# Optimization experiments

Hardware: AMD Instinct MI355X
Metric: run time of the kernel (lower is better)

The kernel has to match this reference:

```python
import jax, jax.numpy as jnp
import numpy as np
from jax import lax

VOCAB = 32000
EMBED = 1024
HIDDEN = 1024
ML = 64          # config.MAX_LENGTH
L = 50           # input sentence length
HH = HIDDEN // 2 # per-direction encoder hidden


def _lstm_cell(x, h, c, Wih, Whh, bih, bhh):
    # torch LSTM gate order: i, f, g, o
    g = x @ Wih.T + h @ Whh.T + bih + bhh
    i, f, gg, o = jnp.split(g, 4)
    i = jax.nn.sigmoid(i)
    f = jax.nn.sigmoid(f)
    gg = jnp.tanh(gg)
    o = jax.nn.sigmoid(o)
    c = f * c + i * gg
    return o * jnp.tanh(c), c


def setup_inputs() -> dict:
    key = jax.random.key(0)
    ks = jax.random.split(key, 24)
    def n(k, shape, s=0.05):
        return jax.random.normal(k, shape, jnp.float32) * s
    return {
        "x_tokens": jax.random.randint(ks[0], (L,), 0, VOCAB, jnp.int32),
        "allowed_mask": jnp.ones((VOCAB + ML,), jnp.float32),
        "embedding": n(ks[1], (VOCAB, EMBED)),
        # encoder bi-LSTM (two cells, each hidden//2)
        "Wih_f": n(ks[2], (4 * HH, EMBED)), "Whh_f": n(ks[3], (4 * HH, HH)),
        "bih_f": n(ks[4], (4 * HH,)), "bhh_f": n(ks[5], (4 * HH,)),
        "Wih_b": n(ks[6], (4 * HH, EMBED)), "Whh_b": n(ks[7], (4 * HH, HH)),
        "bih_b": n(ks[8], (4 * HH,)), "bhh_b": n(ks[9], (4 * HH,)),
        # decoder LSTM: input = embed + 2*hidden
        "Wih_d": n(ks[10], (4 * HIDDEN, EMBED + 2 * HIDDEN)),
        "Whh_d": n(ks[11], (4 * HIDDEN, HIDDEN)),
        "bih_d": n(ks[12], (4 * HIDDEN,)), "bhh_d": n(ks[13], (4 * HIDDEN,)),
        # attention: Linear(2*hidden -> MAX_LENGTH)
        "attn_W": n(ks[14], (ML, 2 * HIDDEN)), "attn_b": n(ks[15], (ML,)),
        # generate layer: Linear(hidden -> vocab)
        "gen_W": n(ks[16], (VOCAB, HIDDEN)), "gen_b": n(ks[17], (VOCAB,)),
        # copy layer: Linear(hidden -> hidden)
        "copy_W": n(ks[18], (HIDDEN, HIDDEN)), "copy_b": n(ks[19], (HIDDEN,)),
    }


def _forward(allowed_mask, embedding, Wih_f, Whh_f, bih_f, bhh_f,
             Wih_b, Whh_b, bih_b, bhh_b, Wih_d, Whh_d, bih_d, bhh_d,
             attn_W, attn_b, gen_W, gen_b, copy_W, copy_b, x_tokens):
    xemb = embedding[x_tokens]  # (L, EMBED)

    # --- encoder: two LSTM cells both stepped forward-in-time (as in the
    # original, where the bidirectional LSTM is called one token at a time) ---
    def enc_step(carry, xe):
        hf, cf, hb, cb = carry
        hf, cf = _lstm_cell(xe, hf, cf, Wih_f, Whh_f, bih_f, bhh_f)
        hb, cb = _lstm_cell(xe, hb, cb, Wih_b, Whh_b, bih_b, bhh_b)
        return (hf, cf, hb, cb), jnp.concatenate([hf, hb])

    z = jnp.zeros((HH,), xemb.dtype)
    (hf, cf, hb, cb), enc = lax.scan(enc_step, (z, z, z, z), xemb)
    enc_outs = jnp.zeros((ML, HIDDEN), xemb.dtype).at[:L].set(enc)  # padded buffer
    h0 = jnp.concatenate([hf, hb])  # (HIDDEN,) decoder init
    c0 = jnp.concatenate([cf, cb])

    copy_enc = jnp.tanh(enc_outs @ copy_W.T + copy_b)  # (ML, HIDDEN), loop-invariant
    pos = jnp.arange(ML)
    sent_pad = jnp.full((ML,), -1, jnp.int32).at[:L].set(x_tokens)
    sos_emb = embedding[0]

    def dec_step(carry, t):
        h, c, prev_probs, prev_word, dec_in = carry
        first = t == 0
        # attentive read
        a = jnp.concatenate([dec_in, h])  # (2*HIDDEN,)
        attw = jax.nn.softmax(a @ attn_W.T + attn_b)
        attentive = attw @ enc_outs  # (HIDDEN,)
        # selective (copy) read from previous step's copy probs
        pc = prev_probs[VOCAB:]
        m = ((pos >= 1) & (pos < L - 1) & (sent_pad != prev_word)).astype(pc.dtype)
        pc = pc * m
        s = pc.sum()
        pc = jnp.where(s > 0, pc / jnp.where(s > 0, s, 1.0), pc)
        selective = pc @ enc_outs
        zero = jnp.zeros_like(attentive)
        attentive = jnp.where(first, zero, attentive)
        selective = jnp.where(first, zero, selective)
        # decoder LSTM step
        h, c = _lstm_cell(jnp.concatenate([dec_in, selective, attentive]),
                          h, c, Wih_d, Whh_d, bih_d, bhh_d)
        gen = h @ gen_W.T + gen_b        # (VOCAB,)
        copy = copy_enc @ h              # (ML,)
        probs = jax.nn.softmax(jnp.concatenate([gen, copy]))
        dist = probs * allowed_mask
        # deterministic action (argmax in place of Categorical.sample)
        aidx = jnp.argmax(dist)
        is_voc = aidx < VOCAB
        src = sent_pad[jnp.clip(aidx - VOCAB, 0, L - 1)]
        action = jnp.where(is_voc, aidx, src).astype(jnp.int32)
        prob = dist[aidx] + jnp.where(
            is_voc, jnp.zeros((), dist.dtype), dist[jnp.clip(action, 0, VOCAB - 1)])
        new = (h, c, lax.stop_gradient(probs), action, embedding[action])
        return new, (h, prob, action)

    carry0 = (h0, c0, jnp.zeros((VOCAB + ML,), h0.dtype),
              jnp.array(-1, jnp.int32), sos_emb)
    _, (hs, probs, actions) = lax.scan(dec_step, carry0, jnp.arange(ML))
    states = jnp.concatenate([h0[None], hs])  # (ML+1, HIDDEN)
    return states, probs, actions


def reference(x_tokens, allowed_mask, embedding, Wih_f, Whh_f, bih_f, bhh_f,
              Wih_b, Whh_b, bih_b, bhh_b, Wih_d, Whh_d, bih_d, bhh_d,
              attn_W, attn_b, gen_W, gen_b, copy_W, copy_b):
    return _forward(allowed_mask, embedding, Wih_f, Whh_f, bih_f, bhh_f,
                    Wih_b, Whh_b, bih_b, bhh_b, Wih_d, Whh_d, bih_d, bhh_d,
                    attn_W, attn_b, gen_W, gen_b, copy_W, copy_b, x_tokens)
```

## Files before the change

kernel.cpp:

```cpp
#include <hip/hip_runtime.h>
#include <math.h>

#define L 50
#define ML 64
#define VOCAB 32000
#define EMBED 1024
#define HID 1024
#define HH 512
#define TOT (VOCAB+ML)
#define NPART 501

#define WS_ENC_GATES 0
#define WS_C_ENC     8192
#define WS_ENC_OUTS  10240
#define WS_COPY_ENC  75776
#define WS_H_DEC     141312
#define WS_C_DEC     143360
#define WS_X_DEC     145408
#define WS_DGATES    148480
#define WS_LOGITS    152576
#define WS_PARTS     184640
#define WS_ATTW      186688
#define WS_PC        186752
#define WS_ACT       186816
#define WS_G         186880
#define WS_G_END     (186880+8192*64)
#define WS_PREG      711168
#define WS_END       (711168+50*4096)

__device__ __forceinline__ float wred_sum(float v){
  #pragma unroll
  for(int o=32;o;o>>=1) v += __shfl_xor(v,o,64);
  return v;
}
__device__ __forceinline__ float wred_max(float v){
  #pragma unroll
  for(int o=32;o;o>>=1) v = fmaxf(v,__shfl_xor(v,o,64));
  return v;
}
__device__ __forceinline__ float sigm(float x){ return 1.0f/(1.0f+__expf(-x)); }
__device__ __forceinline__ float d4(float4 a, float4 b){ return a.x*b.x + a.y*b.y + a.z*b.z + a.w*b.w; }

__global__ __launch_bounds__(256) void k_enc_pre2(
  const int* __restrict__ xt, const float* __restrict__ emb,
  const float* __restrict__ Wih_f, const float* __restrict__ bih_f, const float* __restrict__ bhh_f,
  const float* __restrict__ Wih_b, const float* __restrict__ bih_b, const float* __restrict__ bhh_b,
  float* __restrict__ ws)
{
  __shared__ int toks[L];
  const int tid=threadIdx.x, b=blockIdx.x, wave=tid>>6, lane=tid&63;
  float* pg = ws + WS_PREG;
  if(tid<L) toks[tid]=xt[tid];
  float4 wih[2][4]; float bias[2];
  #pragma unroll
  for(int rr=0;rr<2;rr++){
    int r=b*8+wave*2+rr; bool isF=(r<2048); int rl=isF?r:(r-2048);
    const float* wp=(isF?Wih_f:Wih_b)+(size_t)rl*EMBED;
    #pragma unroll
    for(int c4=0;c4<4;c4++) wih[rr][c4]=*(const float4*)(wp+c4*256+lane*4);
    bias[rr]= isF?(bih_f[rl]+bhh_f[rl]):(bih_b[rl]+bhh_b[rl]);
  }
  __syncthreads();
  for(int t=0;t<L;t++){
    const float* er = emb + (size_t)toks[t]*EMBED;
    #pragma unroll
    for(int rr=0;rr<2;rr++){
      int r=b*8+wave*2+rr;
      float acc=0.0f;
      #pragma unroll
      for(int c4=0;c4<4;c4++) acc += d4(wih[rr][c4], *(const float4*)(er + c4*256 + lane*4));
      acc=wred_sum(acc);
      if(lane==0) pg[(size_t)t*4096+r]=acc+bias[rr];
    }
  }
}

__global__ __launch_bounds__(256) void k_enc_rec(
  const float* __restrict__ Whh_f, const float* __restrict__ Whh_b,
  float* __restrict__ ws, int t)
{
  __shared__ __align__(16) float h_lds[1024];
  const int tid=threadIdx.x, b=blockIdx.x, wave=tid>>6, lane=tid&63;
  float* gates   = ws + WS_ENC_GATES;
  float* c_enc   = ws + WS_C_ENC;
  float* enc_outs= ws + WS_ENC_OUTS;
  const float* pg = ws + WS_PREG + (size_t)t*4096;
  if(t>0){
    const float* gp = gates + ((t-1)&1)*4096;
    const float* cp = c_enc + (t&1)*1024;
    float* cw = c_enc + ((t-1)&1)*1024;
    for(int u=tid;u<1024;u+=256){
      int base=(u<512)?0:2048, uu=(u<512)?u:(u-512);
      float ig=gp[base+uu], fg=gp[base+512+uu], gg=gp[base+1024+uu], og=gp[base+1536+uu];
      float cprev=(t==1)?0.0f:cp[u];
      float c=sigm(fg)*cprev+sigm(ig)*tanhf(gg);
      float h=sigm(og)*tanhf(c);
      h_lds[u]=h;
      if(b==0){ cw[u]=c; enc_outs[(size_t)(t-1)*1024+u]=h; }
    }
  }
  __syncthreads();
  float* gw = gates + (t&1)*4096;
  #pragma unroll
  for(int rr=0;rr<2;rr++){
    int r=b*8+wave*2+rr; bool isF=(r<2048); int rl=isF?r:(r-2048);
    if(t==0){
      if(lane==0) gw[r]=pg[r];
    } else {
      const float* hr=(isF?Whh_f:Whh_b)+(size_t)rl*HH;
      const float* hs=&h_lds[isF?0:512];
      float acc=0.0f;
      #pragma unroll
      for(int c2=0;c2<2;c2++){
        int m=c2*256+lane*4;
        acc += d4(*(const float4*)(hr+m), *(const float4*)(&hs[m]));
      }
      acc=wred_sum(acc);
      if(lane==0) gw[r]=pg[r]+acc;
    }
  }
}

__global__ __launch_bounds__(256) void k_enc_step(
  const int* __restrict__ xt, const float* __restrict__ emb,
  const float* __restrict__ Wih_f, const float* __restrict__ Whh_f,
  const float* __restrict__ bih_f, const float* __restrict__ bhh_f,
  const float* __restrict__ Wih_b, const float* __restrict__ Whh_b,
  const float* __restrict__ bih_b, const float* __restrict__ bhh_b,
  float* __restrict__ ws, int t)
{
  __shared__ __align__(16) float h_lds[1024];
  __shared__ __align__(16) float xe[1024];
  const int tid = threadIdx.x;
  float* gates   = ws + WS_ENC_GATES;
  float* c_enc   = ws + WS_C_ENC;
  float* enc_outs= ws + WS_ENC_OUTS;
  {
    const int tok = xt[t];
    const float* er = emb + (size_t)tok*EMBED;
    for(int j=tid;j<1024;j+=256) xe[j]=er[j];
  }
  if(t>0){
    const float* gp = gates + ((t-1)&1)*4096;
    const float* cp = c_enc + (t&1)*1024;
    float* cw = c_enc + ((t-1)&1)*1024;
    for(int u=tid;u<1024;u+=256){
      int base=(u<512)?0:2048, uu=(u<512)?u:(u-512);
      float ig=gp[base+uu], fg=gp[base+512+uu], gg=gp[base+1024+uu], og=gp[base+1536+uu];
      float cprev=(t==1)?0.0f:cp[u];
      float c=sigm(fg)*cprev+sigm(ig)*tanhf(gg);
      float h=sigm(og)*tanhf(c);
      h_lds[u]=h;
      if(blockIdx.x==0){ cw[u]=c; enc_outs[(size_t)(t-1)*1024+u]=h; }
    }
  }
  __syncthreads();
  float* gw = gates + (t&1)*4096;
  const int wave=tid>>6, lane=tid&63;
  for(int rr=0;rr<2;rr++){
    int r=blockIdx.x*8+wave*2+rr;
    bool isF=(r<2048); int rl=isF?r:(r-2048);
    const float* Wih=isF?Wih_f:Wih_b;
    const float* Whh=isF?Whh_f:Whh_b;
    float bias=isF?(bih_f[rl]+bhh_f[rl]):(bih_b[rl]+bhh_b[rl]);
    const float* wr=Wih+(size_t)rl*EMBED;
    float acc=0.0f;
    #pragma unroll
    for(int c4=0;c4<4;c4++){
      int m=c4*256+lane*4;
      acc += d4(*(const float4*)(wr+m), *(const float4*)(&xe[m]));
    }
    if(t>0){
      const float* hr=Whh+(size_t)rl*HH;
      const float* hs=&h_lds[isF?0:512];
      #pragma unroll
      for(int c2=0;c2<2;c2++){
        int m=c2*256+lane*4;
        acc += d4(*(const float4*)(hr+m), *(const float4*)(&hs[m]));
      }
    }
    acc=wred_sum(acc);
    if(lane==0) gw[r]=acc+bias;
  }
}

__global__ __launch_bounds__(256) void k_copy_final(
  const float* __restrict__ emb,
  const float* __restrict__ copy_W, const float* __restrict__ copy_b,
  float* __restrict__ ws, float* __restrict__ out)
{
  __shared__ __align__(16) float hf[1024];
  const int tid=threadIdx.x, b=blockIdx.x, wave=tid>>6, lane=tid&63;
  float* gates = ws + WS_ENC_GATES;
  float* c_enc = ws + WS_C_ENC;
  float* enc_outs = ws + WS_ENC_OUTS;
  float* cenc = ws + WS_COPY_ENC;
  float* h_dec = ws + WS_H_DEC;
  float* c_dec = ws + WS_C_DEC;
  float* x_dec = ws + WS_X_DEC;
  {
    const float* gp = gates + ((L-1)&1)*4096;
    const float* cp = c_enc + ((L-2)&1)*1024;
    for(int u=tid;u<1024;u+=256){
      int base=(u<512)?0:2048, uu=(u<512)?u:(u-512);
      float ig=gp[base+uu], fg=gp[base+512+uu], gg=gp[base+1024+uu], og=gp[base+1536+uu];
      float c=sigm(fg)*cp[u]+sigm(ig)*tanhf(gg);
      float h=sigm(og)*tanhf(c);
      hf[u]=h;
      if(b==0){
        enc_outs[(size_t)(L-1)*1024+u]=h;
        h_dec[1024+u]=h;
        c_dec[1024+u]=c;
        out[u]=h;
      }
    }
    if(b==1) for(int j=tid;j<(ML-L)*1024;j+=256) enc_outs[(size_t)L*1024+j]=0.0f;
    if(b==2) for(int j=tid;j<1024;j+=256){
      x_dec[j]=emb[j];
      x_dec[1024+j]=0.0f;
      x_dec[2048+j]=0.0f;
    }
  }
  __syncthreads();
  int j = b*4 + wave;
  const float* wr = copy_W + (size_t)j*1024;
  float4 w0=*(const float4*)(wr+0*256+lane*4);
  float4 w1=*(const float4*)(wr+1*256+lane*4);
  float4 w2=*(const float4*)(wr+2*256+lane*4);
  float4 w3=*(const float4*)(wr+3*256+lane*4);
  float bj = copy_b[j];
  for(int k=0;k<L-1;k++){
    const float* er = enc_outs + (size_t)k*1024;
    float acc = d4(w0,*(const float4*)(er+0*256+lane*4))
              + d4(w1,*(const float4*)(er+1*256+lane*4))
              + d4(w2,*(const float4*)(er+2*256+lane*4))
              + d4(w3,*(const float4*)(er+3*256+lane*4));
    acc = wred_sum(acc);
    if(lane==0) cenc[(size_t)k*1024+j]=tanhf(acc+bj);
  }
  {
    float acc = d4(w0,*(const float4*)(&hf[0*256+lane*4]))
              + d4(w1,*(const float4*)(&hf[1*256+lane*4]))
              + d4(w2,*(const float4*)(&hf[2*256+lane*4]))
              + d4(w3,*(const float4*)(&hf[3*256+lane*4]));
    acc = wred_sum(acc);
    if(lane==0) cenc[(size_t)(L-1)*1024+j]=tanhf(acc+bj);
  }
  if(lane==0){
    float z=tanhf(0.0f+bj);
    for(int k=L;k<ML;k++) cenc[(size_t)k*1024+j]=z;
  }
}

__global__ __launch_bounds__(256) void k_gmat(const float* __restrict__ Wih_d, float* __restrict__ ws)
{
  __shared__ __align__(16) float elds[16*1024];
  const int tid=threadIdx.x, wave=tid>>6, lane=tid&63;
  const float* enc = ws + WS_ENC_OUTS;
  float* G = ws + WS_G;
  float4 w[4][4];
  int rg[4];
  #pragma unroll
  for(int q=0;q<4;q++){
    int r = blockIdx.x*16 + wave*4 + q;
    rg[q]=r;
    const float* W = (r<4096) ? (Wih_d + (size_t)r*3072 + 1024)
                              : (Wih_d + (size_t)(r-4096)*3072 + 2048);
    #pragma unroll
    for(int c4=0;c4<4;c4++) w[q][c4]=*(const float4*)(W + c4*256 + lane*4);
  }
  for(int chunk=0;chunk<4;chunk++){
    __syncthreads();
    for(int idx=tid; idx<16*1024; idx+=256) elds[idx]=enc[(size_t)chunk*16*1024+idx];
    __syncthreads();
    for(int k=0;k<16;k++){
      #pragma unroll
      for(int q=0;q<4;q++){
        float acc=0.0f;
        #pragma unroll
        for(int c4=0;c4<4;c4++)
          acc += d4(w[q][c4], *(const float4*)(&elds[k*1024 + c4*256 + lane*4]));
        acc=wred_sum(acc);
        if(lane==0) G[(size_t)rg[q]*64 + chunk*16 + k]=acc;
      }
    }
  }
}

__global__ __launch_bounds__(256) void k_fin16(
  const int* __restrict__ xt, const float* __restrict__ amask,
  const float* __restrict__ emb,
  const float* __restrict__ attn_W, const float* __restrict__ attn_b,
  float* __restrict__ ws, float* __restrict__ out, int t, int fin_only)
{
  __shared__ __align__(16) float dec_in[1024];
  __shared__ __align__(16) float hprev[1024];
  __shared__ float r_lm[256], r_sm[256], r_ky[256];
  __shared__ int r_ix[256];
  __shared__ float s_lmax, s_Z;
  __shared__ int s_act;
  const int tid=threadIdx.x, b=blockIdx.x, wave=tid>>6, lane=tid&63;
  float* h_dec=ws+WS_H_DEC;
  float* logits=ws+WS_LOGITS; float* parts=ws+WS_PARTS;
  float* attw_raw=ws+WS_ATTW; float* pcw=ws+WS_PC;

  {
    float lm=-INFINITY, sm=0.0f, ky=-INFINITY; int ix=0x7fffffff;
    for(int i=tid;i<NPART;i+=256){
      const float4 p = *(const float4*)(parts+(size_t)i*4);
      float plm=p.x, psm=p.y, pky=p.z; int pix=__float_as_int(p.w);
      if(plm>lm){ sm = sm*__expf(lm-plm)+psm; lm=plm; }
      else sm += psm*__expf(plm-lm);
      if(pky>ky || (pky==ky && pix<ix)){ ky=pky; ix=pix; }
    }
    r_lm[tid]=lm; r_sm[tid]=sm; r_ky[tid]=ky; r_ix[tid]=ix;
    __syncthreads();
    for(int s=128;s;s>>=1){
      if(tid<s){
        float blm=r_lm[tid+s], bsm=r_sm[tid+s];
        float alm=r_lm[tid], a_sm=r_sm[tid];
        if(blm>alm){ r_sm[tid]=a_sm*__expf(alm-blm)+bsm; r_lm[tid]=blm; }
        else r_sm[tid]=a_sm+bsm*__expf(blm-alm);
        float bky=r_ky[tid+s]; int bix=r_ix[tid+s];
        if(bky>r_ky[tid] || (bky==r_ky[tid] && bix<r_ix[tid])){ r_ky[tid]=bky; r_ix[tid]=bix; }
      }
      __syncthreads();
    }
    if(tid==0){
      float lmax=r_lm[0]; float Z=r_sm[0];
      float bky=r_ky[0];
      int aidx = (bky==-INFINITY)?0:r_ix[0];
      bool isv = aidx<VOCAB;
      int kcl = aidx-VOCAB; kcl = kcl<0?0:(kcl>(L-1)?(L-1):kcl);
      int sp = xt[kcl];
      int action = isv? aidx : sp;
      if(b==0){
        float prob = amask[aidx]*__expf(logits[aidx]-lmax)/Z;
        if(!isv){
          int a2 = action<0?0:(action>(VOCAB-1)?(VOCAB-1):action);
          prob += amask[a2]*__expf(logits[a2]-lmax)/Z;
        }
        out[65*1024 + (t-1)] = prob;
        out[65*1024 + 64 + (t-1)] = (float)action;
        *(int*)(ws+WS_ACT) = action;
      }
      s_lmax=lmax; s_Z=Z; s_act=action;
    }
  }
  __syncthreads();
  if(fin_only) return;

  const int action = s_act;
  if(b==0 && tid<64){
    int k=tid;
    float v=__expf(logits[VOCAB+k]-s_lmax)/s_Z;
    int sp=(k<L)? xt[k] : -1;
    float m=(k>=1 && k<(L-1) && sp!=action)?1.0f:0.0f;
    float pv=v*m;
    float s=wred_sum(pv);
    pcw[k]=(s>0.0f)? pv/s : pv;
  }
  {
    int row = action<0 ? action+VOCAB : action;
    const float* er = emb + (size_t)row*EMBED;
    const float* hp = h_dec + ((t-1)&1)*1024;
    for(int j=tid;j<1024;j+=256){ dec_in[j]=er[j]; hprev[j]=hp[j]; }
  }
  __syncthreads();
  {
    int r = b*4 + wave;
    const float* wr = attn_W + (size_t)r*2048;
    float acc=0.0f;
    #pragma unroll
    for(int c4=0;c4<4;c4++){
      int m=c4*256+lane*4;
      acc += d4(*(const float4*)(wr+m),      *(const float4*)(&dec_in[m]));
      acc += d4(*(const float4*)(wr+1024+m), *(const float4*)(&hprev[m]));
    }
    acc=wred_sum(acc);
    if(lane==0) attw_raw[r]=acc+attn_b[r];
  }
}

__global__ __launch_bounds__(256) void k_dec_gates3(
  const float* __restrict__ emb,
  const float* __restrict__ Wih_d, const float* __restrict__ Whh_d,
  const float* __restrict__ bih_d, const float* __restrict__ bhh_d,
  float* __restrict__ ws, int t)
{
  __shared__ __align__(16) float di[1024];
  __shared__ __align__(16) float hh[1024];
  __shared__ float pcs[64], aws[64];
  const int tid=threadIdx.x;
  float* h_dec=ws+WS_H_DEC; float* dg=ws+WS_DGATES;
  const float* G=ws+WS_G;
  if(t==0){
    for(int j=tid;j<1024;j+=256) di[j]=emb[j];
    if(tid<64){ pcs[tid]=0.0f; aws[tid]=0.0f; }
  } else {
    const int action = *(const int*)(ws+WS_ACT);
    const float* er = emb + (size_t)action*EMBED;
    for(int j=tid;j<1024;j+=256) di[j]=er[j];
    if(tid<64){
      pcs[tid]=(ws+WS_PC)[tid];
      float v=(ws+WS_ATTW)[tid];
      float mx=wred_max(v);
      float e=__expf(v-mx);
      float s=wred_sum(e);
      aws[tid]=e/s;
    }
  }
  {
    const float* hp=h_dec+((t+1)&1)*1024;
    for(int j=tid;j<1024;j+=256) hh[j]=hp[j];
  }
  __syncthreads();
  const int wave=tid>>6, lane=tid&63;
  for(int rr=0;rr<2;rr++){
    int r=blockIdx.x*8+wave*2+rr;
    const float* wd=Wih_d+(size_t)r*3072;
    float acc=0.0f;
    #pragma unroll
    for(int c4=0;c4<4;c4++){
      int m=c4*256+lane*4;
      acc += d4(*(const float4*)(wd+m), *(const float4*)(&di[m]));
    }
    const float* hr=Whh_d+(size_t)r*1024;
    #pragma unroll
    for(int c4=0;c4<4;c4++){
      int m=c4*256+lane*4;
      acc += d4(*(const float4*)(hr+m), *(const float4*)(&hh[m]));
    }
    acc += G[(size_t)r*64+lane]*pcs[lane];
    acc += G[(size_t)(4096+r)*64+lane]*aws[lane];
    acc=wred_sum(acc);
    if(lane==0) dg[r]=acc+bih_d[r]+bhh_d[r];
  }
}

__global__ __launch_bounds__(256) void k_dec_init(const float* __restrict__ emb, float* __restrict__ ws)
{
  float* x_dec=ws+WS_X_DEC;
  for(int j=threadIdx.x;j<1024;j+=256){
    x_dec[j]=emb[j];
    x_dec[1024+j]=0.0f;
    x_dec[2048+j]=0.0f;
  }
}

__global__ __launch_bounds__(256) void k_attn(
  const int* __restrict__ xt, const float* __restrict__ amask,
  const float* __restrict__ emb,
  const float* __restrict__ attn_W, const float* __restrict__ attn_b,
  float* __restrict__ ws, float* __restrict__ out, int t, int fin_only)
{
  __shared__ __align__(16) float dec_in[1024];
  __shared__ __align__(16) float hprev[1024];
  __shared__ float r_lm[256], r_sm[256], r_ky[256];
  __shared__ int r_ix[256];
  __shared__ float s_lmax, s_Z;
  __shared__ int s_act;
  const int tid=threadIdx.x;
  float* h_dec=ws+WS_H_DEC; float* x_dec=ws+WS_X_DEC;
  float* logits=ws+WS_LOGITS; float* parts=ws+WS_PARTS;
  float* attw_raw=ws+WS_ATTW; float* pcw=ws+WS_PC;
  {
    float lm=-INFINITY, sm=0.0f, ky=-INFINITY; int ix=0x7fffffff;
    for(int i=tid;i<NPART;i+=256){
      const float4 p = *(const float4*)(parts+(size_t)i*4);
      float plm=p.x, psm=p.y, pky=p.z; int pix=__float_as_int(p.w);
      if(plm>lm){ sm = sm*__expf(lm-plm)+psm; lm=plm; }
      else sm += psm*__expf(plm-lm);
      if(pky>ky || (pky==ky && pix<ix)){ ky=pky; ix=pix; }
    }
    r_lm[tid]=lm; r_sm[tid]=sm; r_ky[tid]=ky; r_ix[tid]=ix;
    __syncthreads();
    for(int s=128;s;s>>=1){
      if(tid<s){
        float blm=r_lm[tid+s], bsm=r_sm[tid+s];
        float alm=r_lm[tid], a_sm=r_sm[tid];
        if(blm>alm){ r_sm[tid]=a_sm*__expf(alm-blm)+bsm; r_lm[tid]=blm; }
        else r_sm[tid]=a_sm+bsm*__expf(blm-alm);
        float bky=r_ky[tid+s]; int bix=r_ix[tid+s];
        if(bky>r_ky[tid] || (bky==r_ky[tid] && bix<r_ix[tid])){ r_ky[tid]=bky; r_ix[tid]=bix; }
      }
      __syncthreads();
    }
    if(tid==0){
      float lmax=r_lm[0]; float Z=r_sm[0];
      float bky=r_ky[0];
      int aidx = (bky==-INFINITY)?0:r_ix[0];
      bool isv = aidx<VOCAB;
      int kcl = aidx-VOCAB; kcl = kcl<0?0:(kcl>(L-1)?(L-1):kcl);
      int sp = xt[kcl];
      int action = isv? aidx : sp;
      if(blockIdx.x==0){
        float prob = amask[aidx]*__expf(logits[aidx]-lmax)/Z;
        if(!isv){
          int a2 = action<0?0:(action>(VOCAB-1)?(VOCAB-1):action);
          prob += amask[a2]*__expf(logits[a2]-lmax)/Z;
        }
        out[65*1024 + (t-1)] = prob;
        out[65*1024 + 64 + (t-1)] = (float)action;
      }
      s_lmax=lmax; s_Z=Z; s_act=action;
    }
  }
  __syncthreads();
  if(fin_only) return;
  const int action = s_act;
  if(blockIdx.x==0 && tid<64){
    int k=tid;
    float v=__expf(logits[VOCAB+k]-s_lmax)/s_Z;
    int sp=(k<L)? xt[k] : -1;
    float m=(k>=1 && k<(L-1) && sp!=action)?1.0f:0.0f;
    float pv=v*m;
    float s=wred_sum(pv);
    pcw[k]=(s>0.0f)? pv/s : pv;
  }
  {
    int row = action<0 ? action+VOCAB : action;
    const float* er = emb + (size_t)row*EMBED;
    const float* hp = h_dec + ((t-1)&1)*1024;
    for(int j=tid;j<1024;j+=256){
      float v=er[j];
      dec_in[j]=v; hprev[j]=hp[j];
      if(blockIdx.x==0) x_dec[j]=v;
    }
  }
  __syncthreads();
  if(tid<64){
    const int lane=tid;
    const float* wr = attn_W + (size_t)blockIdx.x*2048;
    float acc=0.0f;
    #pragma unroll
    for(int c4=0;c4<4;c4++){
      int m=c4*256+lane*4;
      acc += d4(*(const float4*)(wr+m),      *(const float4*)(&dec_in[m]));
      acc += d4(*(const float4*)(wr+1024+m), *(const float4*)(&hprev[m]));
    }
    acc=wred_sum(acc);
    if(lane==0) attw_raw[blockIdx.x]=acc+attn_b[blockIdx.x];
  }
}

__global__ __launch_bounds__(256) void k_prep(float* __restrict__ ws)
{
  __shared__ float attw_s[64], pc_s[64];
  const int tid=threadIdx.x;
  float* enc_outs=ws+WS_ENC_OUTS; float* x_dec=ws+WS_X_DEC;
  float* attw_raw=ws+WS_ATTW; float* pcw=ws+WS_PC;
  if(tid<64){
    float v=attw_raw[tid];
    float mx=wred_max(v);
    float e=__expf(v-mx);
    float s=wred_sum(e);
    attw_s[tid]=e/s;
    pc_s[tid]=pcw[tid];
  }
  __syncthreads();
  int j=blockIdx.x*256+tid;
  float aA=0.0f, aS=0.0f;
  for(int k=0;k<ML;k++){
    float e=enc_outs[(size_t)k*1024+j];
    aA += attw_s[k]*e;
    aS += pc_s[k]*e;
  }
  x_dec[1024+j]=aS;
  x_dec[2048+j]=aA;
}

__global__ __launch_bounds__(256) void k_dec_gates(
  const float* __restrict__ Wih_d, const float* __restrict__ Whh_d,
  const float* __restrict__ bih_d, const float* __restrict__ bhh_d,
  float* __restrict__ ws, int t)
{
  __shared__ __align__(16) float x_lds[4096];
  const int tid=threadIdx.x;
  float* x_dec=ws+WS_X_DEC; float* h_dec=ws+WS_H_DEC; float* dg=ws+WS_DGATES;
  for(int j=tid;j<3072;j+=256) x_lds[j]=x_dec[j];
  {
    const float* hp=h_dec+((t+1)&1)*1024;
    for(int j=tid;j<1024;j+=256) x_lds[3072+j]=hp[j];
  }
  __syncthreads();
  const int wave=tid>>6, lane=tid&63;
  for(int rr=0;rr<2;rr++){
    int r=blockIdx.x*8+wave*2+rr;
    const float* wr=Wih_d+(size_t)r*3072;
    float acc=0.0f;
    #pragma unroll
    for(int c4=0;c4<12;c4++){
      int m=c4*256+lane*4;
      acc += d4(*(const float4*)(wr+m), *(const float4*)(&x_lds[m]));
    }
    const float* hr=Whh_d+(size_t)r*1024;
    #pragma unroll
    for(int c4=0;c4<4;c4++){
      int m=c4*256+lane*4;
      acc += d4(*(const float4*)(hr+m), *(const float4*)(&x_lds[3072+m]));
    }
    acc=wred_sum(acc);
    if(lane==0) dg[r]=acc+bih_d[r]+bhh_d[r];
  }
}

__global__ __launch_bounds__(256) void k_dec_gen(
  const float* __restrict__ gen_W, const float* __restrict__ gen_b,
  const float* __restrict__ amask,
  float* __restrict__ ws, float* __restrict__ out, int t)
{
  __shared__ __align__(16) float h_lds[1024];
  __shared__ float w_lm[4], w_sm[4], w_ky[4];
  __shared__ int w_ix[4];
  const int tid=threadIdx.x;
  float* dg=ws+WS_DGATES;
  float* c_dec=ws+WS_C_DEC; float* h_dec=ws+WS_H_DEC;
  float* logits=ws+WS_LOGITS; float* parts=ws+WS_PARTS;
  float* cenc=ws+WS_COPY_ENC;
  {
    const float* cp=c_dec+((t+1)&1)*1024;
    float* cw=c_dec+(t&1)*1024;
    float* hw=h_dec+(t&1)*1024;
    for(int u=tid;u<1024;u+=256){
      float ig=dg[u], fg=dg[1024+u], gg=dg[2048+u], og=dg[3072+u];
      float c=sigm(fg)*cp[u]+sigm(ig)*tanhf(gg);
      float h=sigm(og)*tanhf(c);
      h_lds[u]=h;
      if(blockIdx.x==0){ cw[u]=c; hw[u]=h; out[(size_t)(t+1)*1024+u]=h; }
    }
  }
  __syncthreads();
  const int wave=tid>>6, lane=tid&63;
  const int b=blockIdx.x;
  const bool isGen=(b<500);
  const int rbase = isGen ? (b*64+wave*16) : (VOCAB+wave*16);
  float lv[16];
  #pragma unroll
  for(int rr=0;rr<16;rr++){
    const float* wr = isGen ? gen_W+(size_t)(rbase+rr)*1024
                            : cenc +(size_t)(rbase-VOCAB+rr)*1024;
    float acc=0.0f;
    #pragma unroll
    for(int c4=0;c4<4;c4++){
      int m=c4*256+lane*4;
      acc += d4(*(const float4*)(wr+m), *(const float4*)(&h_lds[m]));
    }
    acc=wred_sum(acc);
    lv[rr] = isGen ? acc+gen_b[rbase+rr] : acc;
  }
  if(lane==0){
    float lm=-INFINITY, ky=-INFINITY; int ix=0;
    #pragma unroll
    for(int rr=0;rr<16;rr++){
      int gi=rbase+rr;
      logits[gi]=lv[rr];
      lm=fmaxf(lm,lv[rr]);
      float mk=amask[gi];
      float kk = (mk>0.0f)? (lv[rr]+__logf(mk)) : -INFINITY;
      if(kk>ky){ ky=kk; ix=gi; }
    }
    float sm=0.0f;
    #pragma unroll
    for(int rr=0;rr<16;rr++) sm += __expf(lv[rr]-lm);
    w_lm[wave]=lm; w_sm[wave]=sm; w_ky[wave]=ky; w_ix[wave]=ix;
  }
  __syncthreads();
  if(tid==0){
    float lm=w_lm[0], sm=w_sm[0], ky=w_ky[0]; int ix=w_ix[0];
    for(int w=1;w<4;w++){
      float blm=w_lm[w], bsm=w_sm[w];
      if(blm>lm){ sm=sm*__expf(lm-blm)+bsm; lm=blm; }
      else sm += bsm*__expf(blm-lm);
      if(w_ky[w]>ky || (w_ky[w]==ky && w_ix[w]<ix)){ ky=w_ky[w]; ix=w_ix[w]; }
    }
    float4 p; p.x=lm; p.y=sm; p.z=ky; p.w=__int_as_float(ix);
    *(float4*)(parts+(size_t)blockIdx.x*4)=p;
  }
}

extern "C" void kernel_launch(void* const* d_in, const int* in_sizes, int n_in,
                              void* d_out, int out_size, void* d_ws, size_t ws_size,
                              hipStream_t stream)
{
  const int*   xt     = (const int*)d_in[0];
  const float* amask  = (const float*)d_in[1];
  const float* emb    = (const float*)d_in[2];
  const float* Wih_f  = (const float*)d_in[3];
  const float* Whh_f  = (const float*)d_in[4];
  const float* bih_f  = (const float*)d_in[5];
  const float* bhh_f  = (const float*)d_in[6];
  const float* Wih_b  = (const float*)d_in[7];
  const float* Whh_b  = (const float*)d_in[8];
  const float* bih_b  = (const float*)d_in[9];
  const float* bhh_b  = (const float*)d_in[10];
  const float* Wih_d  = (const float*)d_in[11];
  const float* Whh_d  = (const float*)d_in[12];
  const float* bih_d  = (const float*)d_in[13];
  const float* bhh_d  = (const float*)d_in[14];
  const float* attn_W = (const float*)d_in[15];
  const float* attn_b = (const float*)d_in[16];
  const float* gen_W  = (const float*)d_in[17];
  const float* gen_b  = (const float*)d_in[18];
  const float* copy_W = (const float*)d_in[19];
  const float* copy_b = (const float*)d_in[20];
  float* out=(float*)d_out;
  float* ws =(float*)d_ws;

  const bool hasG    = ws_size >= (size_t)WS_G_END*sizeof(float);
  const bool hasPreg = ws_size >= (size_t)WS_END*sizeof(float);

  if(hasPreg){
    k_enc_pre2<<<512,256,0,stream>>>(xt,emb,Wih_f,bih_f,bhh_f,Wih_b,bih_b,bhh_b,ws);
    for(int t=0;t<L;t++)
      k_enc_rec<<<512,256,0,stream>>>(Whh_f,Whh_b,ws,t);
  } else {
    for(int t=0;t<L;t++)
      k_enc_step<<<512,256,0,stream>>>(xt,emb,Wih_f,Whh_f,bih_f,bhh_f,Wih_b,Whh_b,bih_b,bhh_b,ws,t);
  }
  k_copy_final<<<256,256,0,stream>>>(emb,copy_W,copy_b,ws,out);

  if(hasG){
    k_gmat<<<512,256,0,stream>>>(Wih_d,ws);
    k_dec_gates3<<<512,256,0,stream>>>(emb,Wih_d,Whh_d,bih_d,bhh_d,ws,0);
    k_dec_gen   <<<501,256,0,stream>>>(gen_W,gen_b,amask,ws,out,0);
    for(int t=1;t<ML;t++){
      k_fin16     <<<16,256,0,stream>>>(xt,amask,emb,attn_W,attn_b,ws,out,t,0);
      k_dec_gates3<<<512,256,0,stream>>>(emb,Wih_d,Whh_d,bih_d,bhh_d,ws,t);
      k_dec_gen   <<<501,256,0,stream>>>(gen_W,gen_b,amask,ws,out,t);
    }
    k_fin16<<<1,256,0,stream>>>(xt,amask,emb,attn_W,attn_b,ws,out,ML,1);
  } else {
    k_dec_init<<<1,256,0,stream>>>(emb,ws);
    k_dec_gates<<<512,256,0,stream>>>(Wih_d,Whh_d,bih_d,bhh_d,ws,0);
    k_dec_gen  <<<501,256,0,stream>>>(gen_W,gen_b,amask,ws,out,0);
    for(int t=1;t<ML;t++){
      k_attn     <<<64,256,0,stream>>>(xt,amask,emb,attn_W,attn_b,ws,out,t,0);
      k_prep     <<<4,256,0,stream>>>(ws);
      k_dec_gates<<<512,256,0,stream>>>(Wih_d,Whh_d,bih_d,bhh_d,ws,t);
      k_dec_gen  <<<501,256,0,stream>>>(gen_W,gen_b,amask,ws,out,t);
    }
    k_attn<<<1,256,0,stream>>>(xt,amask,emb,attn_W,attn_b,ws,out,ML,1);
  }
}
```

Before: 3.099 ms.

## Precompute attention embedding projections and fuse finalize into decoder gate kernel

Adds a one-time table P of attn_W's embedding half applied to every vocabulary embedding, so each decoder step gets its attention logits by a row lookup plus a hidden-state projection. That projection is computed by an extra block appended to the generator kernel. The argmax/softmax finalize, copy and attention softmax are folded into the gate kernel, removing the per-step finalize launch. G's padded columns are zeroed and their compute skipped. The cost is a large upfront projection over all 32000 embeddings and a big workspace requirement, with a fallback path when the workspace is too small.

```diff
diff --git a/kernel.cpp b/kernel.cpp
--- a/kernel.cpp
+++ b/kernel.cpp
@@ -26,7 +26,10 @@
 #define WS_G         186880
 #define WS_G_END     (186880+8192*64)
 #define WS_PREG      711168
-#define WS_END       (711168+50*4096)
+#define WS_PREG_END  (711168+50*4096)
+#define WS_AH        915968
+#define WS_P         916032
+#define WS_P_END     (916032+32000*64)
 
 __device__ __forceinline__ float wred_sum(float v){
   #pragma unroll
@@ -252,7 +255,7 @@
   }
 }
 
-__global__ __launch_bounds__(256) void k_gmat(const float* __restrict__ Wih_d, float* __restrict__ ws)
+__global__ __launch_bounds__(256) void k_gmat2(const float* __restrict__ Wih_d, float* __restrict__ ws)
 {
   __shared__ __align__(16) float elds[16*1024];
   const int tid=threadIdx.x, wave=tid>>6, lane=tid&63;
@@ -270,10 +273,11 @@
     for(int c4=0;c4<4;c4++) w[q][c4]=*(const float4*)(W + c4*256 + lane*4);
   }
   for(int chunk=0;chunk<4;chunk++){
+    const int nk = (chunk<3)?16:2;
     __syncthreads();
-    for(int idx=tid; idx<16*1024; idx+=256) elds[idx]=enc[(size_t)chunk*16*1024+idx];
+    for(int idx=tid; idx<nk*1024; idx+=256) elds[idx]=enc[(size_t)chunk*16*1024+idx];
     __syncthreads();
-    for(int k=0;k<16;k++){
+    for(int k=0;k<nk;k++){
       #pragma unroll
       for(int q=0;q<4;q++){
         float acc=0.0f;
@@ -283,6 +287,42 @@
         acc=wred_sum(acc);
         if(lane==0) G[(size_t)rg[q]*64 + chunk*16 + k]=acc;
       }
+    }
+  }
+  if(lane==0){
+    #pragma unroll
+    for(int q=0;q<4;q++)
+      for(int kk=50;kk<64;kk++) G[(size_t)rg[q]*64 + kk]=0.0f;
+  }
+}
+
+__global__ __launch_bounds__(1024) void k_pmat(
+  const float* __restrict__ emb, const float* __restrict__ attn_W, float* __restrict__ ws)
+{
+  __shared__ __align__(16) float xe[1024];
+  const int tid=threadIdx.x, wave=tid>>6, lane=tid&63;
+  float* P = ws + WS_P;
+  float4 w[4][4];
+  #pragma unroll
+  for(int q=0;q<4;q++){
+    int r = wave*4+q;
+    const float* wr = attn_W + (size_t)r*2048;
+    #pragma unroll
+    for(int c4=0;c4<4;c4++) w[q][c4]=*(const float4*)(wr + c4*256 + lane*4);
+  }
+  const int w0 = blockIdx.x*64;
+  for(int wv=0;wv<64;wv++){
+    __syncthreads();
+    xe[tid]=emb[(size_t)(w0+wv)*EMBED + tid];
+    __syncthreads();
+    #pragma unroll
+    for(int q=0;q<4;q++){
+      int r = wave*4+q;
+      float acc=0.0f;
+      #pragma unroll
+      for(int c4=0;c4<4;c4++) acc += d4(w[q][c4], *(const float4*)(&xe[c4*256+lane*4]));
+      acc=wred_sum(acc);
+      if(lane==0) P[(size_t)(w0+wv)*64 + r]=acc;
     }
   }
 }
@@ -303,7 +343,6 @@
   float* h_dec=ws+WS_H_DEC;
   float* logits=ws+WS_LOGITS; float* parts=ws+WS_PARTS;
   float* attw_raw=ws+WS_ATTW; float* pcw=ws+WS_PC;
-
   {
     float lm=-INFINITY, sm=0.0f, ky=-INFINITY; int ix=0x7fffffff;
     for(int i=tid;i<NPART;i+=256){
@@ -379,6 +418,120 @@
     }
     acc=wred_sum(acc);
     if(lane==0) attw_raw[r]=acc+attn_b[r];
+  }
+}
+
+__global__ __launch_bounds__(256) void k_dec_gates4(
+  const int* __restrict__ xt, const float* __restrict__ amask,
+  const float* __restrict__ emb, const float* __restrict__ attn_b,
+  const float* __restrict__ Wih_d, const float* __restrict__ Whh_d,
+  const float* __restrict__ bih_d, const float* __restrict__ bhh_d,
+  float* __restrict__ ws, float* __restrict__ out, int t)
+{
+  __shared__ __align__(16) float di[1024];
+  __shared__ __align__(16) float hh[1024];
+  __shared__ float pcs[64], aws[64];
+  __shared__ float r_lm[256], r_sm[256], r_ky[256];
+  __shared__ int r_ix[256];
+  __shared__ float s_lmax, s_Z;
+  __shared__ int s_act;
+  const int tid=threadIdx.x, b=blockIdx.x, wave=tid>>6, lane=tid&63;
+  float* h_dec=ws+WS_H_DEC; float* dg=ws+WS_DGATES;
+  float* logits=ws+WS_LOGITS; float* parts=ws+WS_PARTS;
+  const float* G=ws+WS_G;
+
+  if(t==0){
+    for(int j=tid;j<1024;j+=256) di[j]=emb[j];
+    if(tid<64){ pcs[tid]=0.0f; aws[tid]=0.0f; }
+  } else {
+    float lm=-INFINITY, sm=0.0f, ky=-INFINITY; int ix=0x7fffffff;
+    for(int i=tid;i<NPART;i+=256){
+      const float4 p = *(const float4*)(parts+(size_t)i*4);
+      float plm=p.x, psm=p.y, pky=p.z; int pix=__float_as_int(p.w);
+      if(plm>lm){ sm = sm*__expf(lm-plm)+psm; lm=plm; }
+      else sm += psm*__expf(plm-lm);
+      if(pky>ky || (pky==ky && pix<ix)){ ky=pky; ix=pix; }
+    }
+    r_lm[tid]=lm; r_sm[tid]=sm; r_ky[tid]=ky; r_ix[tid]=ix;
+    __syncthreads();
+    for(int s=128;s;s>>=1){
+      if(tid<s){
+        float blm=r_lm[tid+s], bsm=r_sm[tid+s];
+        float alm=r_lm[tid], a_sm=r_sm[tid];
+        if(blm>alm){ r_sm[tid]=a_sm*__expf(alm-blm)+bsm; r_lm[tid]=blm; }
+        else r_sm[tid]=a_sm+bsm*__expf(blm-alm);
+        float bky=r_ky[tid+s]; int bix=r_ix[tid+s];
+        if(bky>r_ky[tid] || (bky==r_ky[tid] && bix<r_ix[tid])){ r_ky[tid]=bky; r_ix[tid]=bix; }
+      }
+      __syncthreads();
+    }
+    if(tid==0){
+      float lmax=r_lm[0]; float Z=r_sm[0];
+      float bky=r_ky[0];
+      int aidx = (bky==-INFINITY)?0:r_ix[0];
+      bool isv = aidx<VOCAB;
+      int kcl = aidx-VOCAB; kcl = kcl<0?0:(kcl>(L-1)?(L-1):kcl);
+      int sp = xt[kcl];
+      int action = isv? aidx : sp;
+      if(b==0){
+        float prob = amask[aidx]*__expf(logits[aidx]-lmax)/Z;
+        if(!isv){
+          int a2 = action<0?0:(action>(VOCAB-1)?(VOCAB-1):action);
+          prob += amask[a2]*__expf(logits[a2]-lmax)/Z;
+        }
+        out[65*1024 + (t-1)] = prob;
+        out[65*1024 + 64 + (t-1)] = (float)action;
+      }
+      s_lmax=lmax; s_Z=Z; s_act=action;
+    }
+    __syncthreads();
+    const int action = s_act;
+    if(tid<64){
+      int k=tid;
+      float v=__expf(logits[VOCAB+k]-s_lmax)/s_Z;
+      int sp=(k<L)? xt[k] : -1;
+      float m=(k>=1 && k<(L-1) && sp!=action)?1.0f:0.0f;
+      float pv=v*m;
+      float s=wred_sum(pv);
+      pcs[k]=(s>0.0f)? pv/s : pv;
+    }
+    __syncthreads();
+    if(tid<64){
+      float raw = (ws+WS_P)[(size_t)action*64 + tid] + (ws+WS_AH)[tid] + attn_b[tid];
+      float mx=wred_max(raw);
+      float e=__expf(raw-mx);
+      float s=wred_sum(e);
+      aws[tid]=e/s;
+    }
+    {
+      const float* er = emb + (size_t)action*EMBED;
+      for(int j=tid;j<1024;j+=256) di[j]=er[j];
+    }
+  }
+  {
+    const float* hp=h_dec+((t+1)&1)*1024;
+    for(int j=tid;j<1024;j+=256) hh[j]=hp[j];
+  }
+  __syncthreads();
+  for(int rr=0;rr<2;rr++){
+    int r=b*8+wave*2+rr;
+    const float* wd=Wih_d+(size_t)r*3072;
+    float acc=0.0f;
+    #pragma unroll
+    for(int c4=0;c4<4;c4++){
+      int m=c4*256+lane*4;
+      acc += d4(*(const float4*)(wd+m), *(const float4*)(&di[m]));
+    }
+    const float* hr=Whh_d+(size_t)r*1024;
+    #pragma unroll
+    for(int c4=0;c4<4;c4++){
+      int m=c4*256+lane*4;
+      acc += d4(*(const float4*)(hr+m), *(const float4*)(&hh[m]));
+    }
+    acc += G[(size_t)r*64+lane]*pcs[lane];
+    acc += G[(size_t)(4096+r)*64+lane]*aws[lane];
+    acc=wred_sum(acc);
+    if(lane==0) dg[r]=acc+bih_d[r]+bhh_d[r];
   }
 }
 
@@ -438,176 +591,9 @@
   }
 }
 
-__global__ __launch_bounds__(256) void k_dec_init(const float* __restrict__ emb, float* __restrict__ ws)
-{
-  float* x_dec=ws+WS_X_DEC;
-  for(int j=threadIdx.x;j<1024;j+=256){
-    x_dec[j]=emb[j];
-    x_dec[1024+j]=0.0f;
-    x_dec[2048+j]=0.0f;
-  }
-}
-
-__global__ __launch_bounds__(256) void k_attn(
-  const int* __restrict__ xt, const float* __restrict__ amask,
-  const float* __restrict__ emb,
-  const float* __restrict__ attn_W, const float* __restrict__ attn_b,
-  float* __restrict__ ws, float* __restrict__ out, int t, int fin_only)
-{
-  __shared__ __align__(16) float dec_in[1024];
-  __shared__ __align__(16) float hprev[1024];
-  __shared__ float r_lm[256], r_sm[256], r_ky[256];
-  __shared__ int r_ix[256];
-  __shared__ float s_lmax, s_Z;
-  __shared__ int s_act;
-  const int tid=threadIdx.x;
-  float* h_dec=ws+WS_H_DEC; float* x_dec=ws+WS_X_DEC;
-  float* logits=ws+WS_LOGITS; float* parts=ws+WS_PARTS;
-  float* attw_raw=ws+WS_ATTW; float* pcw=ws+WS_PC;
-  {
-    float lm=-INFINITY, sm=0.0f, ky=-INFINITY; int ix=0x7fffffff;
-    for(int i=tid;i<NPART;i+=256){
-      const float4 p = *(const float4*)(parts+(size_t)i*4);
-      float plm=p.x, psm=p.y, pky=p.z; int pix=__float_as_int(p.w);
-      if(plm>lm){ sm = sm*__expf(lm-plm)+psm; lm=plm; }
-      else sm += psm*__expf(plm-lm);
-      if(pky>ky || (pky==ky && pix<ix)){ ky=pky; ix=pix; }
-    }
-    r_lm[tid]=lm; r_sm[tid]=sm; r_ky[tid]=ky; r_ix[tid]=ix;
-    __syncthreads();
-    for(int s=128;s;s>>=1){
-      if(tid<s){
-        float blm=r_lm[tid+s], bsm=r_sm[tid+s];
-        float alm=r_lm[tid], a_sm=r_sm[tid];
-        if(blm>alm){ r_sm[tid]=a_sm*__expf(alm-blm)+bsm; r_lm[tid]=blm; }
-        else r_sm[tid]=a_sm+bsm*__expf(blm-alm);
-        float bky=r_ky[tid+s]; int bix=r_ix[tid+s];
-        if(bky>r_ky[tid] || (bky==r_ky[tid] && bix<r_ix[tid])){ r_ky[tid]=bky; r_ix[tid]=bix; }
-      }
-      __syncthreads();
-    }
-    if(tid==0){
-      float lmax=r_lm[0]; float Z=r_sm[0];
-      float bky=r_ky[0];
-      int aidx = (bky==-INFINITY)?0:r_ix[0];
-      bool isv = aidx<VOCAB;
-      int kcl = aidx-VOCAB; kcl = kcl<0?0:(kcl>(L-1)?(L-1):kcl);
-      int sp = xt[kcl];
-      int action = isv? aidx : sp;
-      if(blockIdx.x==0){
-        float prob = amask[aidx]*__expf(logits[aidx]-lmax)/Z;
-        if(!isv){
-          int a2 = action<0?0:(action>(VOCAB-1)?(VOCAB-1):action);
-          prob += amask[a2]*__expf(logits[a2]-lmax)/Z;
-        }
-        out[65*1024 + (t-1)] = prob;
-        out[65*1024 + 64 + (t-1)] = (float)action;
-      }
-      s_lmax=lmax; s_Z=Z; s_act=action;
-    }
-  }
-  __syncthreads();
-  if(fin_only) return;
-  const int action = s_act;
-  if(blockIdx.x==0 && tid<64){
-    int k=tid;
-    float v=__expf(logits[VOCAB+k]-s_lmax)/s_Z;
-    int sp=(k<L)? xt[k] : -1;
-    float m=(k>=1 && k<(L-1) && sp!=action)?1.0f:0.0f;
-    float pv=v*m;
-    float s=wred_sum(pv);
-    pcw[k]=(s>0.0f)? pv/s : pv;
-  }
-  {
-    int row = action<0 ? action+VOCAB : action;
-    const float* er = emb + (size_t)row*EMBED;
-    const float* hp = h_dec + ((t-1)&1)*1024;
-    for(int j=tid;j<1024;j+=256){
-      float v=er[j];
-      dec_in[j]=v; hprev[j]=hp[j];
-      if(blockIdx.x==0) x_dec[j]=v;
-    }
-  }
-  __syncthreads();
-  if(tid<64){
-    const int lane=tid;
-    const float* wr = attn_W + (size_t)blockIdx.x*2048;
-    float acc=0.0f;
-    #pragma unroll
-    for(int c4=0;c4<4;c4++){
-      int m=c4*256+lane*4;
-      acc += d4(*(const float4*)(wr+m),      *(const float4*)(&dec_in[m]));
-      acc += d4(*(const float4*)(wr+1024+m), *(const float4*)(&hprev[m]));
-    }
-    acc=wred_sum(acc);
-    if(lane==0) attw_raw[blockIdx.x]=acc+attn_b[blockIdx.x];
-  }
-}
-
-__global__ __launch_bounds__(256) void k_prep(float* __restrict__ ws)
-{
-  __shared__ float attw_s[64], pc_s[64];
-  const int tid=threadIdx.x;
-  float* enc_outs=ws+WS_ENC_OUTS; float* x_dec=ws+WS_X_DEC;
-  float* attw_raw=ws+WS_ATTW; float* pcw=ws+WS_PC;
-  if(tid<64){
-    float v=attw_raw[tid];
-    float mx=wred_max(v);
-    float e=__expf(v-mx);
-    float s=wred_sum(e);
-    attw_s[tid]=e/s;
-    pc_s[tid]=pcw[tid];
-  }
-  __syncthreads();
-  int j=blockIdx.x*256+tid;
-  float aA=0.0f, aS=0.0f;
-  for(int k=0;k<ML;k++){
-    float e=enc_outs[(size_t)k*1024+j];
-    aA += attw_s[k]*e;
-    aS += pc_s[k]*e;
-  }
-  x_dec[1024+j]=aS;
-  x_dec[2048+j]=aA;
-}
-
-__global__ __launch_bounds__(256) void k_dec_gates(
-  const float* __restrict__ Wih_d, const float* __restrict__ Whh_d,
-  const float* __restrict__ bih_d, const float* __restrict__ bhh_d,
-  float* __restrict__ ws, int t)
-{
-  __shared__ __align__(16) float x_lds[4096];
-  const int tid=threadIdx.x;
-  float* x_dec=ws+WS_X_DEC; float* h_dec=ws+WS_H_DEC; float* dg=ws+WS_DGATES;
-  for(int j=tid;j<3072;j+=256) x_lds[j]=x_dec[j];
-  {
-    const float* hp=h_dec+((t+1)&1)*1024;
-    for(int j=tid;j<1024;j+=256) x_lds[3072+j]=hp[j];
-  }
-  __syncthreads();
-  const int wave=tid>>6, lane=tid&63;
-  for(int rr=0;rr<2;rr++){
-    int r=blockIdx.x*8+wave*2+rr;
-    const float* wr=Wih_d+(size_t)r*3072;
-    float acc=0.0f;
-    #pragma unroll
-    for(int c4=0;c4<12;c4++){
-      int m=c4*256+lane*4;
-      acc += d4(*(const float4*)(wr+m), *(const float4*)(&x_lds[m]));
-    }
-    const float* hr=Whh_d+(size_t)r*1024;
-    #pragma unroll
-    for(int c4=0;c4<4;c4++){
-      int m=c4*256+lane*4;
-      acc += d4(*(const float4*)(hr+m), *(const float4*)(&x_lds[3072+m]));
-    }
-    acc=wred_sum(acc);
-    if(lane==0) dg[r]=acc+bih_d[r]+bhh_d[r];
-  }
-}
-
-__global__ __launch_bounds__(256) void k_dec_gen(
+__global__ __launch_bounds__(256) void k_dec_gen2(
   const float* __restrict__ gen_W, const float* __restrict__ gen_b,
-  const float* __restrict__ amask,
+  const float* __restrict__ amask, const float* __restrict__ attn_W,
   float* __restrict__ ws, float* __restrict__ out, int t)
 {
   __shared__ __align__(16) float h_lds[1024];
@@ -633,6 +619,22 @@
   __syncthreads();
   const int wave=tid>>6, lane=tid&63;
   const int b=blockIdx.x;
+  if(b==501){
+    float* AH=ws+WS_AH;
+    for(int rr=0;rr<16;rr++){
+      int r=wave*16+rr;
+      const float* wr = attn_W + (size_t)r*2048 + 1024;
+      float acc=0.0f;
+      #pragma unroll
+      for(int c4=0;c4<4;c4++){
+        int m=c4*256+lane*4;
+        acc += d4(*(const float4*)(wr+m), *(const float4*)(&h_lds[m]));
+      }
+      acc=wred_sum(acc);
+      if(lane==0) AH[r]=acc;
+    }
+    return;
+  }
   const bool isGen=(b<500);
   const int rbase = isGen ? (b*64+wave*16) : (VOCAB+wave*16);
   float lv[16];
@@ -675,7 +677,7 @@
       if(w_ky[w]>ky || (w_ky[w]==ky && w_ix[w]<ix)){ ky=w_ky[w]; ix=w_ix[w]; }
     }
     float4 p; p.x=lm; p.y=sm; p.z=ky; p.w=__int_as_float(ix);
-    *(float4*)(parts+(size_t)blockIdx.x*4)=p;
+    *(float4*)(parts+(size_t)b*4)=p;
   }
 }
 
@@ -707,8 +709,8 @@
   float* out=(float*)d_out;
   float* ws =(float*)d_ws;
 
-  const bool hasG    = ws_size >= (size_t)WS_G_END*sizeof(float);
-  const bool hasPreg = ws_size >= (size_t)WS_END*sizeof(float);
+  const bool hasPreg = ws_size >= (size_t)WS_PREG_END*sizeof(float);
+  const bool hasP    = ws_size >= (size_t)WS_P_END*sizeof(float);
 
   if(hasPreg){
     k_enc_pre2<<<512,256,0,stream>>>(xt,emb,Wih_f,bih_f,bhh_f,Wih_b,bih_b,bhh_b,ws);
@@ -719,27 +721,23 @@
       k_enc_step<<<512,256,0,stream>>>(xt,emb,Wih_f,Whh_f,bih_f,bhh_f,Wih_b,Whh_b,bih_b,bhh_b,ws,t);
   }
   k_copy_final<<<256,256,0,stream>>>(emb,copy_W,copy_b,ws,out);
-
-  if(hasG){
-    k_gmat<<<512,256,0,stream>>>(Wih_d,ws);
+  k_gmat2<<<512,256,0,stream>>>(Wih_d,ws);
+
+  if(hasP){
+    k_pmat<<<500,1024,0,stream>>>(emb,attn_W,ws);
+    for(int t=0;t<ML;t++){
+      k_dec_gates4<<<512,256,0,stream>>>(xt,amask,emb,attn_b,Wih_d,Whh_d,bih_d,bhh_d,ws,out,t);
+      k_dec_gen2  <<<502,256,0,stream>>>(gen_W,gen_b,amask,attn_W,ws,out,t);
+    }
+    k_fin16<<<1,256,0,stream>>>(xt,amask,emb,attn_W,attn_b,ws,out,ML,1);
+  } else {
     k_dec_gates3<<<512,256,0,stream>>>(emb,Wih_d,Whh_d,bih_d,bhh_d,ws,0);
-    k_dec_gen   <<<501,256,0,stream>>>(gen_W,gen_b,amask,ws,out,0);
+    k_dec_gen2  <<<501,256,0,stream>>>(gen_W,gen_b,amask,attn_W,ws,out,0);
     for(int t=1;t<ML;t++){
       k_fin16     <<<16,256,0,stream>>>(xt,amask,emb,attn_W,attn_b,ws,out,t,0);
       k_dec_gates3<<<512,256,0,stream>>>(emb,Wih_d,Whh_d,bih_d,bhh_d,ws,t);
-      k_dec_gen   <<<501,256,0,stream>>>(gen_W,gen_b,amask,ws,out,t);
+      k_dec_gen2  <<<501,256,0,stream>>>(gen_W,gen_b,amask,attn_W,ws,out,t);
     }
     k_fin16<<<1,256,0,stream>>>(xt,amask,emb,attn_W,attn_b,ws,out,ML,1);
-  } else {
-    k_dec_init<<<1,256,0,stream>>>(emb,ws);
-    k_dec_gates<<<512,256,0,stream>>>(Wih_d,Whh_d,bih_d,bhh_d,ws,0);
-    k_dec_gen  <<<501,256,0,stream>>>(gen_W,gen_b,amask,ws,out,0);
-    for(int t=1;t<ML;t++){
-      k_attn     <<<64,256,0,stream>>>(xt,amask,emb,attn_W,attn_b,ws,out,t,0);
-      k_prep     <<<4,256,0,stream>>>(ws);
-      k_dec_gates<<<512,256,0,stream>>>(Wih_d,Whh_d,bih_d,bhh_d,ws,t);
-      k_dec_gen  <<<501,256,0,stream>>>(gen_W,gen_b,amask,ws,out,t);
-    }
-    k_attn<<<1,256,0,stream>>>(xt,amask,emb,attn_W,attn_b,ws,out,ML,1);
-  }
-}
+  }
+}
```

New measurement: 3.245 ms. 1.05x slower.
